# Kernel optimization log

Measured on AMD Instinct MI355X. Metric: run time of the kernel, lower is better.

The kernel has to match this reference:

```python
import jax, jax.numpy as jnp
import numpy as np
from jax import lax

B, T, MELS, H, K = 32, 2048, 80, 128, 5
MAX_WORDS, MAX_DUR = 64, 128


def _conv1d(x, w, b):
    # x: [B,C,T], w: [O,I,K]
    y = lax.conv_general_dilated(x, w, (1,), 'SAME',
                                 dimension_numbers=('NCH', 'OIH', 'NCH'))
    return y + b[None, :, None]


def _conv2d(x, w, b):
    # x: [B,C,H,W], w: [O,I,K,K]
    y = lax.conv_general_dilated(x, w, (1, 1), 'SAME',
                                 dimension_numbers=('NCHW', 'OIHW', 'NCHW'))
    return y + b[None, :, None, None]


def setup_inputs() -> dict:
    key = jax.random.key(0)
    ks = jax.random.split(key, 20)
    features = jax.random.normal(ks[0], (B, MELS, T), dtype=jnp.float32)
    # monotone word boundaries in [0, T]; starts = bnds[:, :-1], ends = bnds[:, 1:]
    bnds = jnp.sort(jax.random.randint(ks[1], (B, MAX_WORDS + 1), 0, T), axis=-1)
    word_bounds = jnp.stack([bnds[:, :-1], bnds[:, 1:]], axis=1).astype(jnp.int64)  # [B,2,W]
    word_lengths = jax.random.randint(ks[2], (B,), MAX_WORDS // 2, MAX_WORDS + 1).astype(jnp.int64)
    s = 0.05
    p = {
        'w1': jax.random.normal(ks[3], (H, MELS, K)) * s, 'b1': jnp.zeros((H,)),
        'w2': jax.random.normal(ks[4], (H, H, K)) * s, 'b2': jnp.zeros((H,)),
        'w3': jax.random.normal(ks[5], (H, H, K)) * s, 'b3': jnp.zeros((H,)),
        'cw1': jax.random.normal(ks[6], (H, H, K, K)) * s, 'cb1': jnp.zeros((H,)),
        'cw2': jax.random.normal(ks[7], (H, H, K, K)) * s, 'cb2': jnp.zeros((H,)),
        'lw': jax.random.normal(ks[8], (1, MAX_DUR)) * s, 'lb': jnp.zeros((1,)),
        'cw3': jax.random.normal(ks[9], (1, H, K, K)) * s, 'cb3': jnp.zeros((1,)),
    }
    return {'features': features, 'word_bounds': word_bounds, 'word_lengths': word_lengths, **p}


def _slice_words(emb, word_bounds, word_lengths):
    # emb: [B,H,T] -> padded [B,H,MAX_WORDS,MAX_DUR]
    starts = word_bounds[:, 0, :]                      # [B,W]
    durs = word_bounds[:, 1, :] - starts               # [B,W]
    j = jnp.arange(MAX_DUR)                            # [D]
    idx = starts[:, :, None] + j[None, None, :]        # [B,W,D]
    valid = (j[None, None, :] < durs[:, :, None]) & \
            (jnp.arange(MAX_WORDS)[None, :, None] < word_lengths[:, None, None])
    idx = jnp.clip(idx, 0, emb.shape[-1] - 1)
    gathered = jax.vmap(lambda e, ix: e[:, ix])(emb, idx)  # [B,H,W,D]
    return gathered * valid[:, None, :, :].astype(emb.dtype)


def reference(features, word_bounds, word_lengths,
              w1, b1, w2, b2, w3, b3,
              cw1, cb1, cw2, cb2, lw, lb, cw3, cb3):
    # frame encoder
    x = jax.nn.relu(_conv1d(features, w1, b1))
    x = jax.nn.relu(_conv1d(x, w2, b2))
    emb = _conv1d(x, w3, b3)                           # [B,H,T]
    # ragged word slicing + zero-pad scatter (vectorized gather)
    padded = _slice_words(emb, word_bounds, word_lengths)  # [B,H,W,D]
    # word decoder
    y = jax.nn.relu(_conv2d(padded, cw1, cb1))
    y = jax.nn.relu(_conv2d(y, cw2, cb2))
    y = jax.nn.relu(jnp.einsum('bcwd,od->bcwo', y, lw) + lb)  # Linear over duration dim
    out = _conv2d(y, cw3, cb3)                         # [B,1,W,1]
    return out
```

## Files before the change

kernel.cpp:

```cpp
#include <hip/hip_runtime.h>
#include <hip/hip_bf16.h>

#define BB 32
#define TT 2048
#define MELS 80
#define HH 128
#define WW 64
#define DD 128

using bf16x8 = __attribute__((ext_vector_type(8))) short;
using f32x16 = __attribute__((ext_vector_type(16))) float;
using u16x4  = __attribute__((ext_vector_type(4))) ushort;

#define MFMA(av, bv, acc) acc = __builtin_amdgcn_mfma_f32_32x32x16_bf16(av, bv, acc, 0, 0, 0)

__device__ __forceinline__ ushort bf16b(float f) {
  __hip_bfloat16 h = __float2bfloat16(f);
  return *(ushort*)&h;
}

__device__ __forceinline__ void g2l16(const ushort* g, ushort* l) {
  __builtin_amdgcn_global_load_lds((const __attribute__((address_space(1))) void*)g,
                                   (__attribute__((address_space(3))) void*)l, 16, 0, 0);
}

__device__ __forceinline__ void dump_tile(const f32x16& a, int tl, int mb, int half,
                                          const float* __restrict__ bias, bool relu,
                                          ushort* s_y) {
  #pragma unroll
  for (int q = 0; q < 4; ++q) {
    int ho0 = mb + 8 * q + 4 * half;
    u16x4 p;
    #pragma unroll
    for (int j = 0; j < 4; ++j) {
      float v = a[q * 4 + j] + bias[ho0 + j];
      if (relu) v = fmaxf(v, 0.f);
      p[j] = bf16b(v);
    }
    *(u16x4*)&s_y[tl * 128 + (((ho0 >> 3) ^ (tl & 15)) << 3) + (ho0 & 7)] = p;
  }
}

__global__ __launch_bounds__(256) void prep_all(
    const float* __restrict__ features,
    const float* __restrict__ w1, const float* __restrict__ w2,
    const float* __restrict__ w3, const float* __restrict__ cw1,
    const float* __restrict__ cw2, const float* __restrict__ cb1,
    const float* __restrict__ lw,
    ushort* __restrict__ ft, ushort* __restrict__ Wb1, ushort* __restrict__ Wb2,
    ushort* __restrict__ Wb3, ushort* __restrict__ Wc1, ushort* __restrict__ Wc2,
    float* __restrict__ T2, float* __restrict__ Ls, ushort* __restrict__ zp,
    ushort* __restrict__ cvp) {
  __shared__ float s[MELS][65];
  const int bb = blockIdx.x, tid = threadIdx.x;
  if (bb < 1024) {
    const int b = bb >> 5, t0 = (bb & 31) * 64;
    for (int i = tid; i < MELS * 64; i += 256) {
      int c = i >> 6, t = i & 63;
      s[c][t] = features[(b * MELS + c) * TT + t0 + t];
    }
    __syncthreads();
    for (int i = tid; i < 64 * 128; i += 256) {
      int t = i >> 7, c = i & 127;
      float v = (c < MELS) ? s[c][t] : 0.f;
      ft[(b * TT + t0 + t) * 128 + c] = bf16b(v);
    }
  } else if (bb < 1864) {
    int rel, NSS, C; const float* w; ushort* Wb;
    if (bb < 1224)      { rel = bb - 1024; NSS = 5; C = MELS; w = w1; Wb = Wb1; }
    else if (bb < 1544) { rel = bb - 1224; NSS = 8; C = HH;   w = w2; Wb = Wb2; }
    else                { rel = bb - 1544; NSS = 8; C = HH;   w = w3; Wb = Wb3; }
    int i = rel * 256 + tid;
    int e = i & 7, m = (i >> 3) & 127, half = (i >> 10) & 1;
    int r = i >> 11;
    int ss = r % NSS, kw = r / NSS;
    int c = ss * 16 + half * 8 + e;
    Wb[i] = bf16b(w[(m * C + c) * 5 + kw]);
  } else if (bb < 5064) {
    int rel; const float* cw; ushort* Wc;
    if (bb < 3464) { rel = bb - 1864; cw = cw1; Wc = Wc1; }
    else           { rel = bb - 3464; cw = cw2; Wc = Wc2; }
    int i = rel * 256 + tid;
    int e = i & 7, m = (i >> 3) & 127, half = (i >> 10) & 1, ss = (i >> 11) & 7;
    int r = i >> 14;
    int kw = r % 5, kd = r / 5;
    int hi = ss * 16 + half * 8 + e;
    Wc[i] = bf16b(cw[((m * HH + hi) * 5 + kw) * 5 + kd]);
  } else if (bb < 5067) {
    int i = (bb - 5064) * 256 + tid;
    if (i < 640) {
      int ho = i / 5, kw = i - ho * 5;
      float sA = 0.f, sB = 0.f, sC = 0.f;
      for (int hi = 0; hi < HH; ++hi) {
        float yc = fmaxf(cb1[hi], 0.f);
        const float* p = cw2 + ((ho * HH + hi) * 5 + kw) * 5;
        float c012 = p[0] + p[1] + p[2];
        sC += c012 * yc;
        sB += (c012 + p[3]) * yc;
        sA += (c012 + p[3] + p[4]) * yc;
      }
      T2[i * 3 + 0] = sA; T2[i * 3 + 1] = sB; T2[i * 3 + 2] = sC;
    } else if (i < 645) {
      int c = i - 640;
      float sv = 0.f;
      for (int d = c * 32; d < 128; ++d) sv += lw[d];
      Ls[c] = sv;
    }
  } else {
    *(bf16x8*)(zp + tid * 8) = (short)0;
    if (tid < 128) cvp[tid] = bf16b(fmaxf(cb1[tid], 0.f));
  }
}

template<int NSS, int RELU, int D>
__global__ __launch_bounds__(256) void conv1d_mfma(
    const ushort* __restrict__ xt, const ushort* __restrict__ Wb,
    const float* __restrict__ bias, ushort* __restrict__ yt,
    const ushort* __restrict__ zp, const int* __restrict__ wb,
    const int* __restrict__ wlen) {
  __shared__ __align__(16) ushort s_x[1088 * 8];
  const int bid = blockIdx.x;
  const int nid = (bid & 7) * 128 + (bid >> 3);
  const int b = nid >> 5;
  const int t0 = (nid & 31) << 6;
  const int wlb = wlen[b];
  const int lo = wb[b * 128];
  const int hi = wb[b * 128 + 64 + wlb - 1];
  if (t0 >= hi + D || t0 + 64 <= lo - D) return;
  const int tid = threadIdx.x;
  const int lane = tid & 63, wv = tid >> 6;
  const int l31 = lane & 31, half = lane >> 5;
  const int m_w = (wv >> 1) * 64, n32 = (wv & 1) * 32;

  #pragma unroll
  for (int it = 0; it < 5; ++it) {
    int slot = it * 256 + tid;
    if (slot < 1088) {
      int row = slot >> 4, bsw = (slot & 15) ^ (row & 15);
      int t = t0 + row - 2;
      const ushort* src = ((unsigned)t < TT)
          ? xt + (((size_t)(b * TT + t)) << 7) + bsw * 8 : zp;
      g2l16(src, s_x + slot * 8);
    }
  }
  __syncthreads();

  f32x16 a0 = 0.f, a1 = 0.f;
  const bf16x8* Ap = (const bf16x8*)Wb;
  constexpr int G = 5 * NSS;
  #pragma unroll
  for (int g = 0; g < G; ++g) {
    const int kw = g / NSS, ss = g % NSS;
    int r0 = n32 + l31 + kw;
    int blk = ss * 2 + half;
    bf16x8 bv = *(const bf16x8*)&s_x[r0 * 128 + ((blk ^ (r0 & 15)) << 3)];
    int ai = ((kw * NSS + ss) * 2 + half) * 128 + m_w + l31;
    MFMA(Ap[ai],      bv, a0);
    MFMA(Ap[ai + 32], bv, a1);
  }
  __syncthreads();
  dump_tile(a0, n32 + l31, m_w,      half, bias, RELU != 0, s_x);
  dump_tile(a1, n32 + l31, m_w + 32, half, bias, RELU != 0, s_x);
  __syncthreads();
  #pragma unroll
  for (int it = 0; it < 4; ++it) {
    int i = it * 256 + tid;
    int tl = i >> 4, blk = i & 15;
    bf16x8 v = *(const bf16x8*)&s_x[tl * 128 + ((blk ^ (tl & 15)) << 3)];
    *(bf16x8*)(yt + (((size_t)(b * TT + t0 + tl)) << 7) + blk * 8) = v;
  }
}

#define COMPUTE2D(KW, BUF, NB)                                                 \
  {                                                                            \
    bf16x8 ar[2][8];                                                           \
    _Pragma("unroll")                                                          \
    for (int j = 0; j < 8; ++j)                                                \
      ar[0][j] = Ap[(((0 * 5 + (KW)) * 8 + (j >> 1)) * 2 + half) * 128 +       \
                    m_w + l31 + (j & 1) * 32];                                 \
    __builtin_amdgcn_s_setprio(1);                                             \
    _Pragma("unroll")                                                          \
    for (int g = 0; g < 10; ++g) {                                             \
      int kd = g >> 1, sh = (g & 1) * 4;                                       \
      if (g < 9) {                                                             \
        int kd2 = (g + 1) >> 1, sh2 = ((g + 1) & 1) * 4;                       \
        _Pragma("unroll")                                                      \
        for (int j = 0; j < 8; ++j)                                            \
          ar[(g + 1) & 1][j] = Ap[(((kd2 * 5 + (KW)) * 8 + sh2 + (j >> 1)) * 2 \
                                   + half) * 128 + m_w + l31 + (j & 1) * 32];  \
      }                                                                        \
      _Pragma("unroll")                                                        \
      for (int s2 = 0; s2 < 4; ++s2) {                                         \
        int ss = sh + s2;                                                      \
        int r0 = n_w + l31 + kd;                                               \
        int blk = ss * 2 + half;                                               \
        bf16x8 bv0 = *(const bf16x8*)&(BUF)[r0 * 128 + ((blk ^ (r0 & 15)) << 3)]; \
        MFMA(ar[g & 1][s2 * 2],     bv0, a00);                                 \
        MFMA(ar[g & 1][s2 * 2 + 1], bv0, a10);                                 \
        if ((NB) > 1) {                                                        \
          int r1 = r0 + 32;                                                    \
          bf16x8 bv1 = *(const bf16x8*)&(BUF)[r1 * 128 + ((blk ^ (r1 & 15)) << 3)]; \
          MFMA(ar[g & 1][s2 * 2],     bv1, a01);                               \
          MFMA(ar[g & 1][s2 * 2 + 1], bv1, a11);                               \
        }                                                                      \
      }                                                                        \
    }                                                                          \
    __builtin_amdgcn_s_setprio(0);                                             \
  }

__global__ __launch_bounds__(256, 4) void conv2d1_mfma(
    const ushort* __restrict__ embt, const int* __restrict__ wb,
    const int* __restrict__ wlen, const ushort* __restrict__ Wc,
    const float* __restrict__ cb, ushort* __restrict__ y1t,
    const ushort* __restrict__ zp) {
  extern __shared__ __align__(16) ushort smem[];
  const int bid = blockIdx.x;
  const int nid = (bid & 7) * 256 + (bid >> 3);
  const int b = nid >> 6, w = nid & 63;
  const int tid = threadIdx.x;
  const int lane = tid & 63, wv = tid >> 6;
  const int l31 = lane & 31, half = lane >> 5;
  const int m_w = (wv >> 1) * 64, n_w = (wv & 1) * 64;

  int stv[5], duv[5];
  const int wl = wlen[b];
  #pragma unroll
  for (int i = 0; i < 5; ++i) {
    int wq = w + i - 2;
    bool ok = ((unsigned)wq < WW) && (wq < wl);
    int st = ok ? wb[b * 128 + wq] : 0;
    int en = ok ? wb[b * 128 + 64 + wq] : 0;
    stv[i] = st;
    duv[i] = ok ? min(en - st, 128) : 0;
  }
  int dcap = 0;
  #pragma unroll
  for (int i = 0; i < 5; ++i) dcap = max(dcap, duv[i]);
  const int NT1 = min(4, max(1, (dcap + 2 + 31) >> 5));
  const int rstage = min(132, NT1 * 32 + 4);
  const int t0a = n_w >> 5;
  const bool act0 = t0a < NT1, act1 = t0a + 1 < NT1;

#define STAGE1(KW)                                                             \
  {                                                                            \
    const int st_ = stv[KW], du_ = duv[KW];                                    \
    if (du_ > 0) {                                                             \
      const int rs_ = min(rstage, (((du_ + 33) >> 5) << 5) + 4);               \
      _Pragma("unroll")                                                        \
      for (int it = 0; it < 9; ++it) {                                         \
        int slot = it * 256 + tid;                                             \
        if (slot < 2112) {                                                     \
          int row = slot >> 4;                                                 \
          if (row < rs_) {                                                     \
            int bsw = (slot & 15) ^ (row & 15);                                \
            int dq = row - 2;                                                  \
            const ushort* src = ((unsigned)dq < (unsigned)du_)                 \
                ? embt + (((size_t)(b * TT + st_ + dq)) << 7) + bsw * 8 : zp;  \
            g2l16(src, smem + slot * 8);                                       \
          }                                                                    \
        }                                                                      \
      }                                                                        \
    }                                                                          \
  }

  f32x16 a00 = 0.f, a01 = 0.f, a10 = 0.f, a11 = 0.f;
  const bf16x8* Ap = (const bf16x8*)Wc;

  STAGE1(0);
  __syncthreads();
  #pragma unroll
  for (int kw = 0; kw < 5; ++kw) {
    const int du = duv[kw];
    const bool a1k = act1 && (du + 2 > n_w + 32);
    const bool a0k = act0 && (du > 0) && (du + 2 > n_w);
    if (a1k)      { COMPUTE2D(kw, smem, 2); }
    else if (a0k) { COMPUTE2D(kw, smem, 1); }
    __syncthreads();
    if (kw < 4) {
      switch (kw + 1) {
        case 1: STAGE1(1); break;
        case 2: STAGE1(2); break;
        case 3: STAGE1(3); break;
        case 4: STAGE1(4); break;
      }
      __syncthreads();
    }
  }
#undef STAGE1

  if (act0) {
    dump_tile(a00, n_w + l31, m_w,      half, cb, true, smem);
    dump_tile(a10, n_w + l31, m_w + 32, half, cb, true, smem);
  }
  if (act1) {
    dump_tile(a01, n_w + 32 + l31, m_w,      half, cb, true, smem);
    dump_tile(a11, n_w + 32 + l31, m_w + 32, half, cb, true, smem);
  }
  __syncthreads();
  #pragma unroll
  for (int it = 0; it < 8; ++it) {
    int i = it * 256 + tid;
    int d = i >> 4, blk = i & 15;
    if (d < NT1 * 32) {
      bf16x8 v = *(const bf16x8*)&smem[d * 128 + ((blk ^ (d & 15)) << 3)];
      *(bf16x8*)(y1t + (((size_t)(b * WW + w) * DD + d) << 7) + blk * 8) = v;
    }
  }
}

__global__ __launch_bounds__(256, 4) void conv2d2_mfma(
    const ushort* __restrict__ y1t, const int* __restrict__ wb,
    const int* __restrict__ wlen, const ushort* __restrict__ Wc,
    const float* __restrict__ cb, const float* __restrict__ lw,
    const float* __restrict__ lb, const float* __restrict__ T2,
    const float* __restrict__ Ls, float* __restrict__ z,
    const ushort* __restrict__ zp, const ushort* __restrict__ cvp) {
  extern __shared__ __align__(16) ushort smem[];
  const int bid = blockIdx.x;
  const int nid = (bid & 7) * 256 + (bid >> 3);
  const int b = nid >> 6, w = nid & 63;
  const int tid = threadIdx.x;
  const int lane = tid & 63, wv = tid >> 6;
  const int l31 = lane & 31, half = lane >> 5;
  const int m_w = (wv >> 1) * 64, n_w = (wv & 1) * 64;

  int duq[9];
  int dmax = 0;
  const int wl = wlen[b];
  #pragma unroll
  for (int i = 0; i < 9; ++i) {
    int wq = w + i - 4;
    int du = 0;
    if ((unsigned)wq < WW && wq < wl)
      du = min(wb[b * 128 + 64 + wq] - wb[b * 128 + wq], 128);
    duq[i] = du;
    dmax = max(dmax, du);
  }
  const int NT2 = min(4, max(1, (dmax + 4 + 31) >> 5));
  const int rstage = min(132, NT2 * 32 + 4);
  const int t0a = n_w >> 5;
  const bool act0 = t0a < NT2, act1 = t0a + 1 < NT2;

#define STAGE2(KW)                                                             \
  {                                                                            \
    const int wq_ = w + (KW) - 2;                                              \
    if ((unsigned)wq_ < WW) {                                                  \
      int dc_ = 0;                                                             \
      _Pragma("unroll")                                                        \
      for (int m5 = 0; m5 < 5; ++m5) dc_ = max(dc_, duq[(KW) + m5]);           \
      const int lim_ = min(4, max(1, (dc_ + 33) >> 5)) << 5;   \
      _Pragma("unroll")                                                        \
      for (int it = 0; it < 9; ++it) {                                         \
        int slot = it * 256 + tid;                                             \
        if (slot < 2112) {                                                     \
          int row = slot >> 4;                                                 \
          if (row < rstage) {                                                  \
            int bsw = (slot & 15) ^ (row & 15);                                \
            int dq = row - 2;                                                  \
            const ushort* src;                                                 \
            if ((unsigned)dq < (unsigned)lim_)                                 \
              src = y1t + (((size_t)(b * WW + wq_) * DD + dq) << 7) + bsw * 8; \
            else if ((unsigned)dq < (unsigned)DD)                              \
              src = cvp + bsw * 8;                                             \
            else                                                               \
              src = zp;                                                        \
            g2l16(src, smem + slot * 8);                                       \
          }                                                                    \
        }                                                                      \
      }                                                                        \
    }                                                                          \
  }

  f32x16 a00 = 0.f, a01 = 0.f, a10 = 0.f, a11 = 0.f;
  const bf16x8* Ap = (const bf16x8*)Wc;

  STAGE2(0);
  __syncthreads();
  #pragma unroll
  for (int kw = 0; kw < 5; ++kw) {
    const bool kok = (unsigned)(w + kw - 2) < WW;
    if (kok && act1)      { COMPUTE2D(kw, smem, 2); }
    else if (kok && act0) { COMPUTE2D(kw, smem, 1); }
    __syncthreads();
    if (kw < 4) {
      switch (kw + 1) {
        case 1: STAGE2(1); break;
        case 2: STAGE2(2); break;
        case 3: STAGE2(3); break;
        case 4: STAGE2(4); break;
      }
      __syncthreads();
    }
  }
#undef STAGE2

  float* s_red = (float*)smem;
  const float lw0 = lw[n_w + l31], lw1 = lw[n_w + 32 + l31];
  #pragma unroll
  for (int r = 0; r < 16; ++r) {
    int rowoff = (r & 3) + 8 * (r >> 2) + 4 * half;
    {
      int ho = m_w + rowoff;
      float c = cb[ho];
      float v = (act0 ? fmaxf(a00[r] + c, 0.f) * lw0 : 0.f)
              + (act1 ? fmaxf(a01[r] + c, 0.f) * lw1 : 0.f);
      v += __shfl_xor(v, 1); v += __shfl_xor(v, 2); v += __shfl_xor(v, 4);
      v += __shfl_xor(v, 8); v += __shfl_xor(v, 16);
      if (l31 == 0) s_red[ho * 2 + (wv & 1)] = v;
    }
    {
      int ho = m_w + 32 + rowoff;
      float c = cb[ho];
      float v = (act0 ? fmaxf(a10[r] + c, 0.f) * lw0 : 0.f)
              + (act1 ? fmaxf(a11[r] + c, 0.f) * lw1 : 0.f);
      v += __shfl_xor(v, 1); v += __shfl_xor(v, 2); v += __shfl_xor(v, 4);
      v += __shfl_xor(v, 8); v += __shfl_xor(v, 16);
      if (l31 == 0) s_red[ho * 2 + (wv & 1)] = v;
    }
  }
  __syncthreads();
  if (tid < HH) {
    int ho = tid;
    float hiv = 0.f;
    if (NT2 < 4) {
      float ccA = 0.f, ccB = 0.f, ccC = 0.f;
      #pragma unroll
      for (int kw = 0; kw < 5; ++kw) {
        int wq = w + kw - 2;
        if ((unsigned)wq < WW) {
          ccA += T2[(ho * 5 + kw) * 3 + 0];
          ccB += T2[(ho * 5 + kw) * 3 + 1];
          ccC += T2[(ho * 5 + kw) * 3 + 2];
        }
      }
      float c = cb[ho];
      float l126 = lw[126], l127 = lw[127];
      hiv = fmaxf(ccA + c, 0.f) * (Ls[NT2] - l126 - l127)
          + fmaxf(ccB + c, 0.f) * l126
          + fmaxf(ccC + c, 0.f) * l127;
    }
    float zz = fmaxf(s_red[ho * 2] + s_red[ho * 2 + 1] + hiv + lb[0], 0.f);
    z[(b * HH + ho) * WW + w] = zz;
  }
}

__global__ __launch_bounds__(256) void final_k(const float* __restrict__ z,
        const float* __restrict__ cw3, const float* __restrict__ cb3,
        float* __restrict__ out) {
  __shared__ float sred[4][64];
  const int b = blockIdx.x;
  const int tid = threadIdx.x;
  const int w = tid & 63, g = tid >> 6;
  float acc = 0.f;
  for (int hi = g * 32; hi < g * 32 + 32; ++hi) {
    const float* zp_ = z + (b * HH + hi) * WW;
    const float* cp = cw3 + hi * 25 + 2;
    #pragma unroll
    for (int kw = 0; kw < 5; ++kw) {
      int ww = w + kw - 2;
      if ((unsigned)ww < WW) acc += cp[kw * 5] * zp_[ww];
    }
  }
  sred[g][w] = acc;
  __syncthreads();
  if (tid < 64)
    out[b * WW + w] = cb3[0] + sred[0][w] + sred[1][w] + sred[2][w] + sred[3][w];
}

extern "C" void kernel_launch(void* const* d_in, const int* in_sizes, int n_in,
                              void* d_out, int out_size, void* d_ws, size_t ws_size,
                              hipStream_t stream) {
  const float* features = (const float*)d_in[0];
  const int*   wbnd     = (const int*)d_in[1];
  const int*   wlen     = (const int*)d_in[2];
  const float* w1  = (const float*)d_in[3];
  const float* b1  = (const float*)d_in[4];
  const float* w2  = (const float*)d_in[5];
  const float* b2  = (const float*)d_in[6];
  const float* w3  = (const float*)d_in[7];
  const float* b3  = (const float*)d_in[8];
  const float* cw1 = (const float*)d_in[9];
  const float* cb1 = (const float*)d_in[10];
  const float* cw2 = (const float*)d_in[11];
  const float* cb2 = (const float*)d_in[12];
  const float* lw  = (const float*)d_in[13];
  const float* lb  = (const float*)d_in[14];
  const float* cw3 = (const float*)d_in[15];
  const float* cb3 = (const float*)d_in[16];
  float* out = (float*)d_out;

  char* ws = (char*)d_ws;
  ushort* ft   = (ushort*)(ws + 0);
  ushort* x1t  = (ushort*)(ws + 16777216);
  ushort* x2t  = (ushort*)(ws + 33554432);
  ushort* embt = (ushort*)(ws + 0);
  ushort* y1t  = (ushort*)(ws + 16777216);
  float*  z    = (float*)(ws + 83886080);
  ushort* Wb1  = (ushort*)(ws + 84934656);
  ushort* Wb2  = (ushort*)(ws + 85037056);
  ushort* Wb3  = (ushort*)(ws + 85200896);
  ushort* Wc1  = (ushort*)(ws + 85364736);
  ushort* Wc2  = (ushort*)(ws + 86183936);
  ushort* zp   = (ushort*)(ws + 87003136);
  float*  T2   = (float*)(ws + 87007232);
  float*  Ls   = (float*)(ws + 87014912);
  ushort* cvp  = (ushort*)(ws + 87015424);

  const int DYN = 16896 * 2;
  hipFuncSetAttribute((const void*)conv2d1_mfma,
                      hipFuncAttributeMaxDynamicSharedMemorySize, DYN);
  hipFuncSetAttribute((const void*)conv2d2_mfma,
                      hipFuncAttributeMaxDynamicSharedMemorySize, DYN);

  prep_all<<<5068, 256, 0, stream>>>(features, w1, w2, w3, cw1, cw2, cb1, lw,
                                     ft, Wb1, Wb2, Wb3, Wc1, Wc2, T2, Ls, zp, cvp);
  conv1d_mfma<5, 1, 4><<<1024, 256, 0, stream>>>(ft, Wb1, b1, x1t, zp, wbnd, wlen);
  conv1d_mfma<8, 1, 2><<<1024, 256, 0, stream>>>(x1t, Wb2, b2, x2t, zp, wbnd, wlen);
  conv1d_mfma<8, 0, 0><<<1024, 256, 0, stream>>>(x2t, Wb3, b3, embt, zp, wbnd, wlen);
  conv2d1_mfma<<<BB * WW, 256, DYN, stream>>>(embt, wbnd, wlen, Wc1, cb1, y1t, zp);
  conv2d2_mfma<<<BB * WW, 256, DYN, stream>>>(y1t, wbnd, wlen, Wc2, cb2, lw, lb,
                                              T2, Ls, z, zp, cvp);
  final_k<<<BB, 256, 0, stream>>>(z, cw3, cb3, out);
}
```

Measured before the change: 331.1 us.

## Repartition MFMA warp tiles so each wave owns 32 output channels across all time tiles

Each of the four waves now owns a 32-row slice of output channels and loops over up to four 32-wide duration/time tiles, instead of the previous 2x2 split into 64 channels by 64 positions. Work per wave now follows the actual word duration (ntk tiles), so short words do less work, and all four waves stay busy rather than half of them idling on short tiles. Weight fragment loads per wave are halved. The conv1d kernel also gets a three-deep register prefetch of weights with scheduling barriers. The cost is more accumulator registers (four f32x16 tiles) and more LDS B-operand reads per weight fragment, which may pressure occupancy under launch_bounds(256,4).

```diff
diff --git a/kernel.cpp b/kernel.cpp
--- a/kernel.cpp
+++ b/kernel.cpp
@@ -130,7 +130,7 @@
   const int tid = threadIdx.x;
   const int lane = tid & 63, wv = tid >> 6;
   const int l31 = lane & 31, half = lane >> 5;
-  const int m_w = (wv >> 1) * 64, n32 = (wv & 1) * 32;
+  const int wv32 = wv * 32;
 
   #pragma unroll
   for (int it = 0; it < 5; ++it) {
@@ -148,19 +148,27 @@
   f32x16 a0 = 0.f, a1 = 0.f;
   const bf16x8* Ap = (const bf16x8*)Wb;
   constexpr int G = 5 * NSS;
+  bf16x8 ar[3];
+  ar[0] = Ap[(0 * 2 + half) * 128 + wv32 + l31];
+  ar[1] = Ap[(1 * 2 + half) * 128 + wv32 + l31];
+  __builtin_amdgcn_sched_barrier(0);
   #pragma unroll
   for (int g = 0; g < G; ++g) {
+    if (g + 2 < G) {
+      ar[(g + 2) % 3] = Ap[((g + 2) * 2 + half) * 128 + wv32 + l31];
+      __builtin_amdgcn_sched_barrier(0);
+    }
     const int kw = g / NSS, ss = g % NSS;
-    int r0 = n32 + l31 + kw;
+    int r0 = l31 + kw, r1 = 32 + l31 + kw;
     int blk = ss * 2 + half;
-    bf16x8 bv = *(const bf16x8*)&s_x[r0 * 128 + ((blk ^ (r0 & 15)) << 3)];
-    int ai = ((kw * NSS + ss) * 2 + half) * 128 + m_w + l31;
-    MFMA(Ap[ai],      bv, a0);
-    MFMA(Ap[ai + 32], bv, a1);
-  }
-  __syncthreads();
-  dump_tile(a0, n32 + l31, m_w,      half, bias, RELU != 0, s_x);
-  dump_tile(a1, n32 + l31, m_w + 32, half, bias, RELU != 0, s_x);
+    bf16x8 bv0 = *(const bf16x8*)&s_x[r0 * 128 + ((blk ^ (r0 & 15)) << 3)];
+    bf16x8 bv1 = *(const bf16x8*)&s_x[r1 * 128 + ((blk ^ (r1 & 15)) << 3)];
+    MFMA(ar[g % 3], bv0, a0);
+    MFMA(ar[g % 3], bv1, a1);
+  }
+  __syncthreads();
+  dump_tile(a0, l31,      wv32, half, bias, RELU != 0, s_x);
+  dump_tile(a1, 32 + l31, wv32, half, bias, RELU != 0, s_x);
   __syncthreads();
   #pragma unroll
   for (int it = 0; it < 4; ++it) {
@@ -171,13 +179,12 @@
   }
 }
 
-#define COMPUTE2D(KW, BUF, NB)                                                 \
+#define COMPUTE2D(KW, BUF, NTK)                                                \
   {                                                                            \
-    bf16x8 ar[2][8];                                                           \
+    bf16x8 ar[2][4];                                                           \
     _Pragma("unroll")                                                          \
-    for (int j = 0; j < 8; ++j)                                                \
-      ar[0][j] = Ap[(((0 * 5 + (KW)) * 8 + (j >> 1)) * 2 + half) * 128 +       \
-                    m_w + l31 + (j & 1) * 32];                                 \
+    for (int j = 0; j < 4; ++j)                                                \
+      ar[0][j] = Ap[(((0 * 5 + (KW)) * 8 + j) * 2 + half) * 128 + wv32 + l31]; \
     __builtin_amdgcn_s_setprio(1);                                             \
     _Pragma("unroll")                                                          \
     for (int g = 0; g < 10; ++g) {                                             \
@@ -185,23 +192,20 @@
       if (g < 9) {                                                             \
         int kd2 = (g + 1) >> 1, sh2 = ((g + 1) & 1) * 4;                       \
         _Pragma("unroll")                                                      \
-        for (int j = 0; j < 8; ++j)                                            \
-          ar[(g + 1) & 1][j] = Ap[(((kd2 * 5 + (KW)) * 8 + sh2 + (j >> 1)) * 2 \
-                                   + half) * 128 + m_w + l31 + (j & 1) * 32];  \
+        for (int j = 0; j < 4; ++j)                                            \
+          ar[(g + 1) & 1][j] = Ap[(((kd2 * 5 + (KW)) * 8 + sh2 + j) * 2        \
+                                   + half) * 128 + wv32 + l31];                \
       }                                                                        \
       _Pragma("unroll")                                                        \
       for (int s2 = 0; s2 < 4; ++s2) {                                         \
-        int ss = sh + s2;                                                      \
-        int r0 = n_w + l31 + kd;                                               \
-        int blk = ss * 2 + half;                                               \
-        bf16x8 bv0 = *(const bf16x8*)&(BUF)[r0 * 128 + ((blk ^ (r0 & 15)) << 3)]; \
-        MFMA(ar[g & 1][s2 * 2],     bv0, a00);                                 \
-        MFMA(ar[g & 1][s2 * 2 + 1], bv0, a10);                                 \
-        if ((NB) > 1) {                                                        \
-          int r1 = r0 + 32;                                                    \
-          bf16x8 bv1 = *(const bf16x8*)&(BUF)[r1 * 128 + ((blk ^ (r1 & 15)) << 3)]; \
-          MFMA(ar[g & 1][s2 * 2],     bv1, a01);                               \
-          MFMA(ar[g & 1][s2 * 2 + 1], bv1, a11);                               \
+        int blk = (sh + s2) * 2 + half;                                        \
+        _Pragma("unroll")                                                      \
+        for (int nj = 0; nj < 4; ++nj) {                                       \
+          if (nj < (NTK)) {                                                    \
+            int r0 = nj * 32 + l31 + kd;                                       \
+            bf16x8 bv = *(const bf16x8*)&(BUF)[r0 * 128 + ((blk ^ (r0 & 15)) << 3)]; \
+            MFMA(ar[g & 1][s2], bv, acc[nj]);                                  \
+          }                                                                    \
         }                                                                      \
       }                                                                        \
     }                                                                          \
@@ -220,7 +224,7 @@
   const int tid = threadIdx.x;
   const int lane = tid & 63, wv = tid >> 6;
   const int l31 = lane & 31, half = lane >> 5;
-  const int m_w = (wv >> 1) * 64, n_w = (wv & 1) * 64;
+  const int wv32 = wv * 32;
 
   int stv[5], duv[5];
   const int wl = wlen[b];
@@ -238,8 +242,6 @@
   for (int i = 0; i < 5; ++i) dcap = max(dcap, duv[i]);
   const int NT1 = min(4, max(1, (dcap + 2 + 31) >> 5));
   const int rstage = min(132, NT1 * 32 + 4);
-  const int t0a = n_w >> 5;
-  const bool act0 = t0a < NT1, act1 = t0a + 1 < NT1;
 
 #define STAGE1(KW)                                                             \
   {                                                                            \
@@ -263,7 +265,9 @@
     }                                                                          \
   }
 
-  f32x16 a00 = 0.f, a01 = 0.f, a10 = 0.f, a11 = 0.f;
+  f32x16 acc[4];
+  #pragma unroll
+  for (int nj = 0; nj < 4; ++nj) acc[nj] = 0.f;
   const bf16x8* Ap = (const bf16x8*)Wc;
 
   STAGE1(0);
@@ -271,10 +275,8 @@
   #pragma unroll
   for (int kw = 0; kw < 5; ++kw) {
     const int du = duv[kw];
-    const bool a1k = act1 && (du + 2 > n_w + 32);
-    const bool a0k = act0 && (du > 0) && (du + 2 > n_w);
-    if (a1k)      { COMPUTE2D(kw, smem, 2); }
-    else if (a0k) { COMPUTE2D(kw, smem, 1); }
+    const int ntk = (du > 0) ? min(4, (du + 33) >> 5) : 0;
+    if (ntk > 0) { COMPUTE2D(kw, smem, ntk); }
     __syncthreads();
     if (kw < 4) {
       switch (kw + 1) {
@@ -288,14 +290,10 @@
   }
 #undef STAGE1
 
-  if (act0) {
-    dump_tile(a00, n_w + l31, m_w,      half, cb, true, smem);
-    dump_tile(a10, n_w + l31, m_w + 32, half, cb, true, smem);
-  }
-  if (act1) {
-    dump_tile(a01, n_w + 32 + l31, m_w,      half, cb, true, smem);
-    dump_tile(a11, n_w + 32 + l31, m_w + 32, half, cb, true, smem);
-  }
+  #pragma unroll
+  for (int nj = 0; nj < 4; ++nj)
+    if (nj < NT1)
+      dump_tile(acc[nj], nj * 32 + l31, wv32, half, cb, true, smem);
   __syncthreads();
   #pragma unroll
   for (int it = 0; it < 8; ++it) {
@@ -322,7 +320,7 @@
   const int tid = threadIdx.x;
   const int lane = tid & 63, wv = tid >> 6;
   const int l31 = lane & 31, half = lane >> 5;
-  const int m_w = (wv >> 1) * 64, n_w = (wv & 1) * 64;
+  const int wv32 = wv * 32;
 
   int duq[9];
   int dmax = 0;
@@ -338,8 +336,6 @@
   }
   const int NT2 = min(4, max(1, (dmax + 4 + 31) >> 5));
   const int rstage = min(132, NT2 * 32 + 4);
-  const int t0a = n_w >> 5;
-  const bool act0 = t0a < NT2, act1 = t0a + 1 < NT2;
 
 #define STAGE2(KW)                                                             \
   {                                                                            \
@@ -371,7 +367,9 @@
     }                                                                          \
   }
 
-  f32x16 a00 = 0.f, a01 = 0.f, a10 = 0.f, a11 = 0.f;
+  f32x16 acc[4];
+  #pragma unroll
+  for (int nj = 0; nj < 4; ++nj) acc[nj] = 0.f;
   const bf16x8* Ap = (const bf16x8*)Wc;
 
   STAGE2(0);
@@ -379,8 +377,8 @@
   #pragma unroll
   for (int kw = 0; kw < 5; ++kw) {
     const bool kok = (unsigned)(w + kw - 2) < WW;
-    if (kok && act1)      { COMPUTE2D(kw, smem, 2); }
-    else if (kok && act0) { COMPUTE2D(kw, smem, 1); }
+    const int ntk = kok ? NT2 : 0;
+    if (ntk > 0) { COMPUTE2D(kw, smem, ntk); }
     __syncthreads();
     if (kw < 4) {
       switch (kw + 1) {
@@ -395,28 +393,20 @@
 #undef STAGE2
 
   float* s_red = (float*)smem;
-  const float lw0 = lw[n_w + l31], lw1 = lw[n_w + 32 + l31];
+  float lwv[4];
+  #pragma unroll
+  for (int nj = 0; nj < 4; ++nj) lwv[nj] = lw[nj * 32 + l31];
   #pragma unroll
   for (int r = 0; r < 16; ++r) {
-    int rowoff = (r & 3) + 8 * (r >> 2) + 4 * half;
-    {
-      int ho = m_w + rowoff;
-      float c = cb[ho];
-      float v = (act0 ? fmaxf(a00[r] + c, 0.f) * lw0 : 0.f)
-              + (act1 ? fmaxf(a01[r] + c, 0.f) * lw1 : 0.f);
-      v += __shfl_xor(v, 1); v += __shfl_xor(v, 2); v += __shfl_xor(v, 4);
-      v += __shfl_xor(v, 8); v += __shfl_xor(v, 16);
-      if (l31 == 0) s_red[ho * 2 + (wv & 1)] = v;
-    }
-    {
-      int ho = m_w + 32 + rowoff;
-      float c = cb[ho];
-      float v = (act0 ? fmaxf(a10[r] + c, 0.f) * lw0 : 0.f)
-              + (act1 ? fmaxf(a11[r] + c, 0.f) * lw1 : 0.f);
-      v += __shfl_xor(v, 1); v += __shfl_xor(v, 2); v += __shfl_xor(v, 4);
-      v += __shfl_xor(v, 8); v += __shfl_xor(v, 16);
-      if (l31 == 0) s_red[ho * 2 + (wv & 1)] = v;
-    }
+    int ho = wv32 + (r & 3) + 8 * (r >> 2) + 4 * half;
+    float c = cb[ho];
+    float v = 0.f;
+    #pragma unroll
+    for (int nj = 0; nj < 4; ++nj)
+      if (nj < NT2) v += fmaxf(acc[nj][r] + c, 0.f) * lwv[nj];
+    v += __shfl_xor(v, 1); v += __shfl_xor(v, 2); v += __shfl_xor(v, 4);
+    v += __shfl_xor(v, 8); v += __shfl_xor(v, 16);
+    if (l31 == 0) s_red[ho] = v;
   }
   __syncthreads();
   if (tid < HH) {
@@ -439,7 +429,7 @@
           + fmaxf(ccB + c, 0.f) * l126
           + fmaxf(ccC + c, 0.f) * l127;
     }
-    float zz = fmaxf(s_red[ho * 2] + s_red[ho * 2 + 1] + hiv + lb[0], 0.f);
+    float zz = fmaxf(s_red[ho] + hiv + lb[0], 0.f);
     z[(b * HH + ho) * WW + w] = zz;
   }
 }
```

New measurement: 343.0 us. 1.04x slower.
